# Performance work log

Measured on AMD Instinct MI355X. Metric: run time of the kernel, lower is better.

## Reference

```python
import jax, jax.numpy as jnp
import numpy as np

A = 4   # tree arity
D = 7   # tree depth; total nodes = (A**D - 1)//(A - 1) = 5461
B = 64  # batch size
E = 128 # embedding_dim
H = 128 # encode_dim
V = 50000
N_NODES = (A**D - 1) // (A - 1)


def setup_inputs() -> dict:
    key = jax.random.key(0)
    ks = jax.random.split(key, 9)
    tokens = jax.random.randint(ks[0], (N_NODES, B), 0, V, dtype=jnp.int64)
    emb = jax.random.normal(ks[1], (V, E), dtype=jnp.float32) * 0.05
    sent_w = jax.random.normal(ks[2], (H, H), dtype=jnp.float32) * 0.05
    sent_b = jax.random.normal(ks[3], (1, H), dtype=jnp.float32) * 0.05
    ctx_w = jax.random.normal(ks[4], (H, 1), dtype=jnp.float32) * 0.05
    w_ih = jax.random.normal(ks[5], (3 * H, E), dtype=jnp.float32) * 0.05
    w_hh = jax.random.normal(ks[6], (3 * H, H), dtype=jnp.float32) * 0.05
    b_ih = jax.random.normal(ks[7], (3 * H,), dtype=jnp.float32) * 0.05
    b_hh = jax.random.normal(ks[8], (3 * H,), dtype=jnp.float32) * 0.05
    return {"tokens": tokens, "emb": emb, "sent_w": sent_w, "sent_b": sent_b,
            "ctx_w": ctx_w, "w_ih": w_ih, "w_hh": w_hh, "b_ih": b_ih, "b_hh": b_hh}


def _gru_step(x, h, w_ih, w_hh, b_ih, b_hh):
    # x: [n, B, E], h: [n, B, H] -> new hidden [n, B, H]. PyTorch gate order r,z,n.
    gi = jnp.einsum('nbe,ge->nbg', x, w_ih) + b_ih   # [n, B, 3H]
    gh = jnp.einsum('nbh,gh->nbg', h, w_hh) + b_hh
    ir, iz, in_ = jnp.split(gi, 3, axis=-1)
    hr, hz, hn_ = jnp.split(gh, 3, axis=-1)
    r = jax.nn.sigmoid(ir + hr)
    z = jax.nn.sigmoid(iz + hz)
    n = jnp.tanh(in_ + r * hn_)
    return (1.0 - z) * n + z * h


def reference(tokens, emb, sent_w, sent_b, ctx_w, w_ih, w_hh, b_ih, b_hh):
    # Bottom-up over tree levels (level-order storage): level d occupies
    # tokens[(A**d-1)//(A-1) : ... + A**d]. Each node position covers the whole batch.
    hs = None       # hiddens of the level below: [A**(d+1), B, H]
    out_max = None  # running elementwise max over all node hiddens (node_list max)
    for d in range(D - 1, -1, -1):
        n = A ** d
        off = (A ** d - 1) // (A - 1)
        tok = tokens[off:off + n]          # [n, B]
        x = emb[tok]                       # [n, B, E]
        if hs is None:
            h0 = jnp.zeros((n, B, H), dtype=emb.dtype)  # leaves: no children
        else:
            ch = hs.reshape(n, A, B, H)    # children hiddens per parent
            # attention: tanh(ch @ W + b), tanh(. @ ctx), softmax over children
            u = jnp.tanh(jnp.einsum('nabh,hk->nabk', ch, sent_w) + sent_b)
            s = jnp.tanh(jnp.einsum('nabk,k->nab', u, ctx_w[:, 0]))  # [n, A, B]
            alpha = jax.nn.softmax(s, axis=1)                        # over A children
            h0 = jnp.einsum('nabh,nab->nbh', ch, alpha)              # weighted sum
        hn = _gru_step(x, h0, w_ih, w_hh, b_ih, b_hh)                # [n, B, H]
        lvl_max = hn.max(axis=0)                                     # [B, H]
        out_max = lvl_max if out_max is None else jnp.maximum(out_max, lvl_max)
        hs = hn
    return out_max  # [B, H]
```

## Files before the change

kernel.cpp:

```cpp
#include <hip/hip_runtime.h>
#include <cstdint>
#include <cstddef>


typedef short  bf16x8 __attribute__((ext_vector_type(8)));
typedef float  f32x4  __attribute__((ext_vector_type(4)));

#define WS_ACC    0u
#define WS_WIH    1048576u
#define WS_WHH    (WS_WIH + 98304u)
#define WS_SWT    (WS_WHH + 98304u)
#define WS_EMBB   (WS_SWT + 32768u)
#define WS_HLEAF  (WS_EMBB + 12800000u)
#define WS_HA     (WS_HLEAF + 12800000u)
#define WS_HB     (WS_HA + 4194304u)

__device__ __forceinline__ float sigm(float x)   { return 1.0f / (1.0f + __expf(-x)); }
__device__ __forceinline__ float tanhf_(float x) { return 1.0f - 2.0f / (1.0f + __expf(2.0f * x)); }

__device__ __forceinline__ unsigned short f2b(float f) {
  unsigned u = __float_as_uint(f);
  u += 0x7fffu + ((u >> 16) & 1u);
  return (unsigned short)(u >> 16);
}
__device__ __forceinline__ float b2f(unsigned short s) {
  return __uint_as_float(((unsigned)s) << 16);
}

__device__ __forceinline__ unsigned fenc(float f) {
  unsigned u = __float_as_uint(f);
  return (u & 0x80000000u) ? ~u : (u | 0x80000000u);
}
__device__ __forceinline__ float fdec(unsigned e) {
  unsigned u = (e & 0x80000000u) ? (e & 0x7fffffffu) : ~e;
  return __uint_as_float(u);
}

__device__ __forceinline__ f32x4 mfma16(bf16x8 a, bf16x8 b, f32x4 c) {
  return __builtin_amdgcn_mfma_f32_16x16x32_bf16(a, b, c, 0, 0, 0);
}

__global__ __launch_bounds__(256) void decode_out(const unsigned* __restrict__ acc,
                                                  float* __restrict__ out) {
  int i = blockIdx.x * 256 + threadIdx.x;
  unsigned m = 0u;
  for (int s = 0; s < 32; ++s) m = max(m, acc[s * 8192 + i]);
  out[i] = fdec(m);
}

__global__ __launch_bounds__(256) void prep_all(const float* __restrict__ emb,
                                                const float* __restrict__ wih,
                                                const float* __restrict__ whh,
                                                const float* __restrict__ sw,
                                                unsigned short* __restrict__ embb,
                                                unsigned short* __restrict__ wihb,
                                                unsigned short* __restrict__ whhb,
                                                unsigned short* __restrict__ swtb,
                                                unsigned* __restrict__ acc) {
  size_t idx = (size_t)blockIdx.x * 256 + threadIdx.x;
  if (idx < 1600000u) {
    float4 v = *(const float4*)(emb + idx * 4);
    ushort4 o; o.x = f2b(v.x); o.y = f2b(v.y); o.z = f2b(v.z); o.w = f2b(v.w);
    *(ushort4*)(embb + idx * 4) = o;
  } else if (idx < 1714688u) {
    int i = (int)(idx - 1600000u);
    if (i < 49152)       wihb[i] = f2b(wih[i]);
    else if (i < 98304)  whhb[i - 49152] = f2b(whh[i - 49152]);
    else { int j = i - 98304; int k = j >> 7, h = j & 127; swtb[j] = f2b(sw[h * 128 + k]); }
  } else {
    acc[idx - 1714688u] = 0u;
  }
}

__global__ __launch_bounds__(512, 2) void prep_hleaf(
    const unsigned short* __restrict__ embb,
    const unsigned short* __restrict__ wih,
    const float*          __restrict__ b_ih,
    const float*          __restrict__ b_hh,
    unsigned short*       __restrict__ H)
{
  __shared__ unsigned short lds[64 * 128];
  __shared__ unsigned short hvb[64 * 128];
  const int t = threadIdx.x;
  const int base = blockIdx.x * 64;

#pragma unroll
  for (int i = 0; i < 2; ++i) {
    int g = t + 512 * i;
    int m = g >> 4, c = g & 15;
    int v = base + m; if (v > 49999) v = 49999;
    uint4 vv = *(const uint4*)(embb + (size_t)v * 128 + c * 8);
    *(uint4*)(lds + m * 128 + ((c ^ (m & 15)) << 3)) = vv;
  }

  const int w = __builtin_amdgcn_readfirstlane(t >> 6);
  const int lane = t & 63, l = lane & 15, q = lane >> 4;
  const int j = w * 16 + l;

  bf16x8 Br[4], Bz[4], Bn[4];
#pragma unroll
  for (int ks = 0; ks < 4; ++ks) {
    const int ko = ks * 32 + q * 8;
    Br[ks] = *(const bf16x8*)(wih + (size_t)j * 128 + ko);
    Bz[ks] = *(const bf16x8*)(wih + (size_t)(128 + j) * 128 + ko);
    Bn[ks] = *(const bf16x8*)(wih + (size_t)(256 + j) * 128 + ko);
  }
  const float bR = b_ih[j] + b_hh[j];
  const float bZ = b_ih[128 + j] + b_hh[128 + j];
  const float bN = b_ih[256 + j];
  const float bH = b_hh[256 + j];

  f32x4 Cr[4] = {{0,0,0,0},{0,0,0,0},{0,0,0,0},{0,0,0,0}};
  f32x4 Cz[4] = {{0,0,0,0},{0,0,0,0},{0,0,0,0},{0,0,0,0}};
  f32x4 Cn[4] = {{0,0,0,0},{0,0,0,0},{0,0,0,0},{0,0,0,0}};
  __syncthreads();

#pragma unroll
  for (int ks = 0; ks < 4; ++ks) {
    bf16x8 A[4];
#pragma unroll
    for (int mt = 0; mt < 4; ++mt) {
      int m = mt * 16 + l, c = ks * 4 + q;
      A[mt] = *(const bf16x8*)(lds + m * 128 + (((c ^ l) & 15) << 3));
    }
#pragma unroll
    for (int mt = 0; mt < 4; ++mt) {
      Cr[mt] = mfma16(A[mt], Br[ks], Cr[mt]);
      Cz[mt] = mfma16(A[mt], Bz[ks], Cz[mt]);
      Cn[mt] = mfma16(A[mt], Bn[ks], Cn[mt]);
    }
  }

#pragma unroll
  for (int mt = 0; mt < 4; ++mt)
#pragma unroll
    for (int e = 0; e < 4; ++e) {
      int b = mt * 16 + q * 4 + e;
      float r  = sigm(Cr[mt][e] + bR);
      float z  = sigm(Cz[mt][e] + bZ);
      float nv = tanhf_(Cn[mt][e] + bN + r * bH);
      float hv = (1.0f - z) * nv;
      hvb[b * 128 + (j ^ (q << 4))] = f2b(hv);
    }
  __syncthreads();

#pragma unroll
  for (int i = 0; i < 2; ++i) {
    int g = t + 512 * i;
    int b = g >> 4, c8 = (g & 15) * 8;
    int qq = (b >> 2) & 3;
    if (base + b < 50000) {
      uint4 v = *(const uint4*)(hvb + b * 128 + (c8 ^ (qq << 4)));
      *(uint4*)(H + (size_t)(base + b) * 128 + c8) = v;
    }
  }
}

template <bool LEAF>
__global__ __launch_bounds__(512, 2) void attn_gru(
    const unsigned short* __restrict__ hch,
    const int*            __restrict__ tokc,
    const unsigned short* __restrict__ hleaf,
    const unsigned short* __restrict__ swt,
    const float*          __restrict__ sb,
    const float*          __restrict__ ctx,
    const int*            __restrict__ tok,
    const unsigned short* __restrict__ embb,
    const unsigned short* __restrict__ wih,
    const unsigned short* __restrict__ whh,
    const float*          __restrict__ b_ih,
    const float*          __restrict__ b_hh,
    unsigned short*       __restrict__ hout,
    unsigned*             __restrict__ acc)
{
  __shared__ unsigned short chs[256 * 128];
  __shared__ float spart[4][256];
  __shared__ float alf[256];
  unsigned short* const atile = chs;
  unsigned short* const hvb   = chs + 16384;

  const int p = blockIdx.x;
  const int t = threadIdx.x;

  const int sm0 = t >> 4,         sc0 = t & 15;
  const int sm1 = (t + 512) >> 4, sc1 = (t + 512) & 15;
  const int* tp = tok + p * 64;
  uint4 px0 = *(const uint4*)(embb + (size_t)tp[sm0] * 128 + sc0 * 8);
  uint4 px1 = *(const uint4*)(embb + (size_t)tp[sm1] * 128 + sc1 * 8);

  if constexpr (LEAF) {
    const int* tokp = tokc + p * 256;
#pragma unroll
    for (int i = 0; i < 8; ++i) {
      int g = t + 512 * i, m = g >> 4, c = g & 15;
      uint4 v = *(const uint4*)(hleaf + (size_t)tokp[m] * 128 + c * 8);
      *(uint4*)(chs + m * 128 + ((c ^ (m & 15)) << 3)) = v;
    }
  } else {
    const unsigned short* src = hch + (size_t)p * 256 * 128;
#pragma unroll
    for (int i = 0; i < 8; ++i) {
      int g = t + 512 * i, m = g >> 4, c = g & 15;
      uint4 v = *(const uint4*)(src + m * 128 + c * 8);
      *(uint4*)(chs + m * 128 + ((c ^ (m & 15)) << 3)) = v;
    }
  }

  const int w = __builtin_amdgcn_readfirstlane(t >> 6);
  const int wm = w >> 2, wn = w & 3;
  const int lane = t & 63, l = lane & 15, q = lane >> 4;
  const int j = w * 16 + l;

  bf16x8 Bs[2][4];
#pragma unroll
  for (int nt = 0; nt < 2; ++nt)
#pragma unroll
    for (int ks = 0; ks < 4; ++ks)
      Bs[nt][ks] = *(const bf16x8*)(swt + (size_t)(wn * 32 + nt * 16 + l) * 128 + ks * 32 + q * 8);

  f32x4 Cu[8][2] = {};
  __syncthreads();

#pragma unroll
  for (int ks = 0; ks < 4; ++ks) {
#pragma unroll
    for (int mt = 0; mt < 8; ++mt) {
      int m = wm * 128 + mt * 16 + l;
      int c = ks * 4 + q;
      bf16x8 A = *(const bf16x8*)(chs + m * 128 + (((c ^ (m & 15)) & 15) << 3));
      Cu[mt][0] = mfma16(A, Bs[0][ks], Cu[mt][0]);
      Cu[mt][1] = mfma16(A, Bs[1][ks], Cu[mt][1]);
    }
  }

  const float sb0 = sb[wn * 32 + l],  sb1 = sb[wn * 32 + 16 + l];
  const float cx0 = ctx[wn * 32 + l], cx1 = ctx[wn * 32 + 16 + l];
#pragma unroll
  for (int mt = 0; mt < 8; ++mt) {
    float pe[4];
#pragma unroll
    for (int e = 0; e < 4; ++e)
      pe[e] = tanhf_(Cu[mt][0][e] + sb0) * cx0 + tanhf_(Cu[mt][1][e] + sb1) * cx1;
#pragma unroll
    for (int mask = 1; mask < 16; mask <<= 1)
#pragma unroll
      for (int e = 0; e < 4; ++e)
        pe[e] += __shfl_xor(pe[e], mask, 16);
    if (l == 0) {
      int r = wm * 128 + mt * 16 + q * 4;
#pragma unroll
      for (int e = 0; e < 4; ++e) spart[wn][r + e] = pe[e];
    }
  }
  __syncthreads();

  if (t < 256) {
    float s = tanhf_(spart[0][t] + spart[1][t] + spart[2][t] + spart[3][t]);
    spart[0][t] = s;
  }
  __syncthreads();
  if (t < 64) {
    float s0 = spart[0][t], s1 = spart[0][64 + t], s2 = spart[0][128 + t], s3 = spart[0][192 + t];
    float m = fmaxf(fmaxf(s0, s1), fmaxf(s2, s3));
    float e0 = __expf(s0 - m), e1 = __expf(s1 - m), e2 = __expf(s2 - m), e3 = __expf(s3 - m);
    float inv = 1.0f / (e0 + e1 + e2 + e3);
    alf[t] = e0 * inv; alf[64 + t] = e1 * inv; alf[128 + t] = e2 * inv; alf[192 + t] = e3 * inv;
  }
  __syncthreads();

  float o[2][8];
#pragma unroll
  for (int i = 0; i < 2; ++i) {
    int id = t + 512 * i, b = id >> 4, c = id & 15;
#pragma unroll
    for (int k = 0; k < 8; ++k) o[i][k] = 0.0f;
#pragma unroll
    for (int a = 0; a < 4; ++a) {
      int m = a * 64 + b;
      const unsigned short* rp = chs + m * 128 + ((c ^ (m & 15)) << 3);
      float al = alf[m];
#pragma unroll
      for (int k = 0; k < 8; ++k) o[i][k] += al * b2f(rp[k]);
    }
  }

  float mxv[16];
  if constexpr (LEAF) {
    const int jj = t & 127, cc = jj >> 3;
#pragma unroll
    for (int e = 0; e < 16; ++e) mxv[e] = -1e30f;
#pragma unroll
    for (int a = 0; a < 4; ++a)
#pragma unroll
      for (int e = 0; e < 16; ++e) {
        int b = (t >> 7) + 4 * e, m = a * 64 + b;
        float v = b2f(chs[m * 128 + (((cc ^ (m & 15)) & 15) << 3) + (jj & 7)]);
        mxv[e] = fmaxf(mxv[e], v);
      }
  }
  __syncthreads();

  *(uint4*)(atile + sm0 * 256 + ((sc0 ^ (sm0 & 15)) << 3)) = px0;
  *(uint4*)(atile + sm1 * 256 + ((sc1 ^ (sm1 & 15)) << 3)) = px1;
#pragma unroll
  for (int i = 0; i < 2; ++i) {
    int id = t + 512 * i, b = id >> 4, c = id & 15;
    ushort4 h0a, h0b4;
    h0a.x = f2b(o[i][0]); h0a.y = f2b(o[i][1]); h0a.z = f2b(o[i][2]); h0a.w = f2b(o[i][3]);
    h0b4.x = f2b(o[i][4]); h0b4.y = f2b(o[i][5]); h0b4.z = f2b(o[i][6]); h0b4.w = f2b(o[i][7]);
    unsigned short* dst = atile + b * 256 + ((16 | ((c ^ (b & 15)) & 15)) << 3);
    *(ushort4*)dst = h0a;
    *(ushort4*)(dst + 4) = h0b4;
  }

  bf16x8 Br[8], Bz[8], Bn[4], Bh[4];
#pragma unroll
  for (int ks = 0; ks < 4; ++ks) {
    const int ko = ks * 32 + q * 8;
    Br[ks]     = *(const bf16x8*)(wih + (size_t)j * 128 + ko);
    Bz[ks]     = *(const bf16x8*)(wih + (size_t)(128 + j) * 128 + ko);
    Bn[ks]     = *(const bf16x8*)(wih + (size_t)(256 + j) * 128 + ko);
    Br[4 + ks] = *(const bf16x8*)(whh + (size_t)j * 128 + ko);
    Bz[4 + ks] = *(const bf16x8*)(whh + (size_t)(128 + j) * 128 + ko);
    Bh[ks]     = *(const bf16x8*)(whh + (size_t)(256 + j) * 128 + ko);
  }
  const float bR = b_ih[j] + b_hh[j];
  const float bZ = b_ih[128 + j] + b_hh[128 + j];
  const float bN = b_ih[256 + j];
  const float bH = b_hh[256 + j];
  __syncthreads();

  f32x4 Cr[4] = {{0,0,0,0},{0,0,0,0},{0,0,0,0},{0,0,0,0}};
  f32x4 Cz[4] = {{0,0,0,0},{0,0,0,0},{0,0,0,0},{0,0,0,0}};
  f32x4 Cn[4] = {{0,0,0,0},{0,0,0,0},{0,0,0,0},{0,0,0,0}};
  f32x4 Ch[4] = {{0,0,0,0},{0,0,0,0},{0,0,0,0},{0,0,0,0}};

#pragma unroll
  for (int ks = 0; ks < 8; ++ks) {
#pragma unroll
    for (int mt = 0; mt < 4; ++mt) {
      int m = mt * 16 + l;
      int c = ks * 4 + q;
      bf16x8 Amt = *(const bf16x8*)(atile + m * 256 + (((c & 16) | ((c ^ l) & 15)) << 3));
      Cr[mt] = mfma16(Amt, Br[ks], Cr[mt]);
      Cz[mt] = mfma16(Amt, Bz[ks], Cz[mt]);
      if (ks < 4) Cn[mt] = mfma16(Amt, Bn[ks], Cn[mt]);
      else        Ch[mt] = mfma16(Amt, Bh[ks - 4], Ch[mt]);
    }
  }

  float mx[4][4];
#pragma unroll
  for (int mt = 0; mt < 4; ++mt) {
#pragma unroll
    for (int e = 0; e < 4; ++e) {
      const int b = mt * 16 + q * 4 + e;
      float r  = sigm(Cr[mt][e] + bR);
      float z  = sigm(Cz[mt][e] + bZ);
      float nv = tanhf_(Cn[mt][e] + bN + r * (Ch[mt][e] + bH));
      int c16 = j >> 3;
      float hp = b2f(atile[b * 256 + ((16 | ((c16 ^ (b & 15)) & 15)) << 3) + (j & 7)]);
      float hv = (1.0f - z) * nv + z * hp;
      hvb[b * 128 + (j ^ (q << 4))] = f2b(hv);
      mx[mt][e] = hv;
    }
  }
  __syncthreads();

  unsigned short* ho = hout + (size_t)p * 8192;
  {
    int c80 = sc0 * 8, q0 = (sm0 >> 2) & 3;
    int c81 = sc1 * 8, q1 = (sm1 >> 2) & 3;
    uint4 v0 = *(const uint4*)(hvb + sm0 * 128 + (c80 ^ (q0 << 4)));
    uint4 v1 = *(const uint4*)(hvb + sm1 * 128 + (c81 ^ (q1 << 4)));
    *(uint4*)(ho + sm0 * 128 + c80) = v0;
    *(uint4*)(ho + sm1 * 128 + c81) = v1;
  }

  unsigned* accs = acc + (p & 31) * 8192;
#pragma unroll
  for (int mt = 0; mt < 4; ++mt)
#pragma unroll
    for (int e = 0; e < 4; ++e) {
      const int b = mt * 16 + q * 4 + e;
      atomicMax(accs + b * 128 + j, fenc(mx[mt][e]));
    }
  if constexpr (LEAF) {
#pragma unroll
    for (int e = 0; e < 16; ++e)
      atomicMax(accs + t + 512 * e, fenc(mxv[e]));
  }
}

extern "C" void kernel_launch(void* const* d_in, const int* in_sizes, int n_in,
                              void* d_out, int out_size, void* d_ws, size_t ws_size,
                              hipStream_t stream) {
  const int*   tokens = (const int*)d_in[0];
  const float* emb    = (const float*)d_in[1];
  const float* sent_w = (const float*)d_in[2];
  const float* sent_b = (const float*)d_in[3];
  const float* ctx_w  = (const float*)d_in[4];
  const float* w_ih   = (const float*)d_in[5];
  const float* w_hh   = (const float*)d_in[6];
  const float* b_ih   = (const float*)d_in[7];
  const float* b_hh   = (const float*)d_in[8];

  char* ws = (char*)d_ws;
  unsigned*       acc  = (unsigned*)(ws + WS_ACC);
  unsigned short* wihb = (unsigned short*)(ws + WS_WIH);
  unsigned short* whhb = (unsigned short*)(ws + WS_WHH);
  unsigned short* swtb = (unsigned short*)(ws + WS_SWT);
  unsigned short* embb = (unsigned short*)(ws + WS_EMBB);
  unsigned short* hlf  = (unsigned short*)(ws + WS_HLEAF);
  unsigned short* hA   = (unsigned short*)(ws + WS_HA);
  unsigned short* hB   = (unsigned short*)(ws + WS_HB);

  hipLaunchKernelGGL(prep_all, dim3(7722), dim3(256), 0, stream,
                     emb, w_ih, w_hh, sent_w, embb, wihb, whhb, swtb, acc);
  hipLaunchKernelGGL(prep_hleaf, dim3(782), dim3(512), 0, stream,
                     embb, wihb, b_ih, b_hh, hlf);

  static const int offs[7] = {0, 1, 5, 21, 85, 341, 1365};
  const int* tok6 = tokens + (size_t)1365 * 64;

  for (int d = 5; d >= 0; --d) {
    int n = 1 << (2 * d);
    unsigned short* hout  = (d & 1) ? hB : hA;
    unsigned short* child = (d & 1) ? hA : hB;
    if (d == 5) {
      hipLaunchKernelGGL((attn_gru<true>), dim3(n), dim3(512), 0, stream,
                         (const unsigned short*)nullptr, tok6, hlf,
                         swtb, sent_b, ctx_w,
                         tokens + (size_t)offs[5] * 64, embb, wihb, whhb,
                         b_ih, b_hh, hout, acc);
    } else {
      hipLaunchKernelGGL((attn_gru<false>), dim3(n), dim3(512), 0, stream,
                         child, (const int*)nullptr, (const unsigned short*)nullptr,
                         swtb, sent_b, ctx_w,
                         tokens + (size_t)offs[d] * 64, embb, wihb, whhb,
                         b_ih, b_hh, hout, acc);
    }
  }
  hipLaunchKernelGGL(decode_out, dim3(32), dim3(256), 0, stream, acc, (float*)d_out);
}
```

Baseline: 350.5 us.

## Split each tree node's batch across two blocks and raise occupancy

Each attn_gru block now handles half of the 64-wide batch for one parent node, which doubles the grid and halves the shared-memory tile (256x128 down to 128x128 bf16). Launch bounds go from 2 to 4 blocks per CU, and the GRU weight fragments are streamed with a one-step register prefetch instead of all being held in registers. The goal is more parallelism on the small upper tree levels and higher occupancy to hide memory latency. In exchange, the W_ih/W_hh and attention weights are reloaded by twice as many blocks, and register limits under the higher occupancy target could cause spills.

```diff
diff --git a/kernel.cpp b/kernel.cpp
--- a/kernel.cpp
+++ b/kernel.cpp
@@ -157,7 +157,7 @@
 }
 
 template <bool LEAF>
-__global__ __launch_bounds__(512, 2) void attn_gru(
+__global__ __launch_bounds__(512, 4) void attn_gru(
     const unsigned short* __restrict__ hch,
     const int*            __restrict__ tokc,
     const unsigned short* __restrict__ hleaf,
@@ -173,35 +173,35 @@
     unsigned short*       __restrict__ hout,
     unsigned*             __restrict__ acc)
 {
-  __shared__ unsigned short chs[256 * 128];
-  __shared__ float spart[4][256];
-  __shared__ float alf[256];
+  __shared__ unsigned short chs[128 * 128];
+  __shared__ float spart[4][128];
+  __shared__ float alf[128];
   unsigned short* const atile = chs;
-  unsigned short* const hvb   = chs + 16384;
-
-  const int p = blockIdx.x;
+  unsigned short* const hvb   = chs + 8192;
+
+  const int p2 = blockIdx.x;
+  const int p = p2 >> 1, half = p2 & 1;
   const int t = threadIdx.x;
 
-  const int sm0 = t >> 4,         sc0 = t & 15;
-  const int sm1 = (t + 512) >> 4, sc1 = (t + 512) & 15;
-  const int* tp = tok + p * 64;
-  uint4 px0 = *(const uint4*)(embb + (size_t)tp[sm0] * 128 + sc0 * 8);
-  uint4 px1 = *(const uint4*)(embb + (size_t)tp[sm1] * 128 + sc1 * 8);
+  const int sm = t >> 4, sc = t & 15;
+  const int* tp = tok + p * 64 + half * 32;
+  uint4 px = *(const uint4*)(embb + (size_t)tp[sm] * 128 + sc * 8);
 
   if constexpr (LEAF) {
     const int* tokp = tokc + p * 256;
 #pragma unroll
-    for (int i = 0; i < 8; ++i) {
+    for (int i = 0; i < 4; ++i) {
       int g = t + 512 * i, m = g >> 4, c = g & 15;
-      uint4 v = *(const uint4*)(hleaf + (size_t)tokp[m] * 128 + c * 8);
+      int bg = (m >> 5) * 64 + half * 32 + (m & 31);
+      uint4 v = *(const uint4*)(hleaf + (size_t)tokp[bg] * 128 + c * 8);
       *(uint4*)(chs + m * 128 + ((c ^ (m & 15)) << 3)) = v;
     }
   } else {
-    const unsigned short* src = hch + (size_t)p * 256 * 128;
-#pragma unroll
-    for (int i = 0; i < 8; ++i) {
+#pragma unroll
+    for (int i = 0; i < 4; ++i) {
       int g = t + 512 * i, m = g >> 4, c = g & 15;
-      uint4 v = *(const uint4*)(src + m * 128 + c * 8);
+      int bg = (m >> 5) * 64 + half * 32 + (m & 31);
+      uint4 v = *(const uint4*)(hch + ((size_t)p * 256 + bg) * 128 + c * 8);
       *(uint4*)(chs + m * 128 + ((c ^ (m & 15)) << 3)) = v;
     }
   }
@@ -218,14 +218,14 @@
     for (int ks = 0; ks < 4; ++ks)
       Bs[nt][ks] = *(const bf16x8*)(swt + (size_t)(wn * 32 + nt * 16 + l) * 128 + ks * 32 + q * 8);
 
-  f32x4 Cu[8][2] = {};
+  f32x4 Cu[4][2] = {};
   __syncthreads();
 
 #pragma unroll
   for (int ks = 0; ks < 4; ++ks) {
 #pragma unroll
-    for (int mt = 0; mt < 8; ++mt) {
-      int m = wm * 128 + mt * 16 + l;
+    for (int mt = 0; mt < 4; ++mt) {
+      int m = wm * 64 + mt * 16 + l;
       int c = ks * 4 + q;
       bf16x8 A = *(const bf16x8*)(chs + m * 128 + (((c ^ (m & 15)) & 15) << 3));
       Cu[mt][0] = mfma16(A, Bs[0][ks], Cu[mt][0]);
@@ -236,7 +236,7 @@
   const float sb0 = sb[wn * 32 + l],  sb1 = sb[wn * 32 + 16 + l];
   const float cx0 = ctx[wn * 32 + l], cx1 = ctx[wn * 32 + 16 + l];
 #pragma unroll
-  for (int mt = 0; mt < 8; ++mt) {
+  for (int mt = 0; mt < 4; ++mt) {
     float pe[4];
 #pragma unroll
     for (int e = 0; e < 4; ++e)
@@ -247,111 +247,110 @@
       for (int e = 0; e < 4; ++e)
         pe[e] += __shfl_xor(pe[e], mask, 16);
     if (l == 0) {
-      int r = wm * 128 + mt * 16 + q * 4;
+      int r = wm * 64 + mt * 16 + q * 4;
 #pragma unroll
       for (int e = 0; e < 4; ++e) spart[wn][r + e] = pe[e];
     }
   }
   __syncthreads();
 
-  if (t < 256) {
-    float s = tanhf_(spart[0][t] + spart[1][t] + spart[2][t] + spart[3][t]);
-    spart[0][t] = s;
-  }
-  __syncthreads();
-  if (t < 64) {
-    float s0 = spart[0][t], s1 = spart[0][64 + t], s2 = spart[0][128 + t], s3 = spart[0][192 + t];
-    float m = fmaxf(fmaxf(s0, s1), fmaxf(s2, s3));
-    float e0 = __expf(s0 - m), e1 = __expf(s1 - m), e2 = __expf(s2 - m), e3 = __expf(s3 - m);
+  if (t < 32) {
+    float sv[4];
+#pragma unroll
+    for (int a = 0; a < 4; ++a) {
+      int r = a * 32 + t;
+      sv[a] = tanhf_(spart[0][r] + spart[1][r] + spart[2][r] + spart[3][r]);
+    }
+    float m = fmaxf(fmaxf(sv[0], sv[1]), fmaxf(sv[2], sv[3]));
+    float e0 = __expf(sv[0] - m), e1 = __expf(sv[1] - m);
+    float e2 = __expf(sv[2] - m), e3 = __expf(sv[3] - m);
     float inv = 1.0f / (e0 + e1 + e2 + e3);
-    alf[t] = e0 * inv; alf[64 + t] = e1 * inv; alf[128 + t] = e2 * inv; alf[192 + t] = e3 * inv;
-  }
-  __syncthreads();
-
-  float o[2][8];
-#pragma unroll
-  for (int i = 0; i < 2; ++i) {
-    int id = t + 512 * i, b = id >> 4, c = id & 15;
-#pragma unroll
-    for (int k = 0; k < 8; ++k) o[i][k] = 0.0f;
+    alf[t] = e0 * inv; alf[32 + t] = e1 * inv; alf[64 + t] = e2 * inv; alf[96 + t] = e3 * inv;
+  }
+  __syncthreads();
+
+  float o[8] = {0, 0, 0, 0, 0, 0, 0, 0};
+  {
+    int rb = t >> 4, c = t & 15;
 #pragma unroll
     for (int a = 0; a < 4; ++a) {
-      int m = a * 64 + b;
+      int m = a * 32 + rb;
       const unsigned short* rp = chs + m * 128 + ((c ^ (m & 15)) << 3);
       float al = alf[m];
 #pragma unroll
-      for (int k = 0; k < 8; ++k) o[i][k] += al * b2f(rp[k]);
-    }
-  }
-
-  float mxv[16];
+      for (int k = 0; k < 8; ++k) o[k] += al * b2f(rp[k]);
+    }
+  }
+
+  float mxv[8];
   if constexpr (LEAF) {
     const int jj = t & 127, cc = jj >> 3;
 #pragma unroll
-    for (int e = 0; e < 16; ++e) mxv[e] = -1e30f;
+    for (int e = 0; e < 8; ++e) mxv[e] = -1e30f;
 #pragma unroll
     for (int a = 0; a < 4; ++a)
 #pragma unroll
-      for (int e = 0; e < 16; ++e) {
-        int b = (t >> 7) + 4 * e, m = a * 64 + b;
+      for (int e = 0; e < 8; ++e) {
+        int rb = (t >> 7) + 4 * e, m = a * 32 + rb;
         float v = b2f(chs[m * 128 + (((cc ^ (m & 15)) & 15) << 3) + (jj & 7)]);
         mxv[e] = fmaxf(mxv[e], v);
       }
   }
   __syncthreads();
 
-  *(uint4*)(atile + sm0 * 256 + ((sc0 ^ (sm0 & 15)) << 3)) = px0;
-  *(uint4*)(atile + sm1 * 256 + ((sc1 ^ (sm1 & 15)) << 3)) = px1;
-#pragma unroll
-  for (int i = 0; i < 2; ++i) {
-    int id = t + 512 * i, b = id >> 4, c = id & 15;
-    ushort4 h0a, h0b4;
-    h0a.x = f2b(o[i][0]); h0a.y = f2b(o[i][1]); h0a.z = f2b(o[i][2]); h0a.w = f2b(o[i][3]);
-    h0b4.x = f2b(o[i][4]); h0b4.y = f2b(o[i][5]); h0b4.z = f2b(o[i][6]); h0b4.w = f2b(o[i][7]);
-    unsigned short* dst = atile + b * 256 + ((16 | ((c ^ (b & 15)) & 15)) << 3);
-    *(ushort4*)dst = h0a;
-    *(ushort4*)(dst + 4) = h0b4;
-  }
-
-  bf16x8 Br[8], Bz[8], Bn[4], Bh[4];
-#pragma unroll
-  for (int ks = 0; ks < 4; ++ks) {
-    const int ko = ks * 32 + q * 8;
-    Br[ks]     = *(const bf16x8*)(wih + (size_t)j * 128 + ko);
-    Bz[ks]     = *(const bf16x8*)(wih + (size_t)(128 + j) * 128 + ko);
-    Bn[ks]     = *(const bf16x8*)(wih + (size_t)(256 + j) * 128 + ko);
-    Br[4 + ks] = *(const bf16x8*)(whh + (size_t)j * 128 + ko);
-    Bz[4 + ks] = *(const bf16x8*)(whh + (size_t)(128 + j) * 128 + ko);
-    Bh[ks]     = *(const bf16x8*)(whh + (size_t)(256 + j) * 128 + ko);
-  }
+  *(uint4*)(atile + sm * 256 + ((sc ^ (sm & 15)) << 3)) = px;
+  {
+    int rb = t >> 4, c = t & 15;
+    ushort4 ha, hb;
+    ha.x = f2b(o[0]); ha.y = f2b(o[1]); ha.z = f2b(o[2]); ha.w = f2b(o[3]);
+    hb.x = f2b(o[4]); hb.y = f2b(o[5]); hb.z = f2b(o[6]); hb.w = f2b(o[7]);
+    unsigned short* dst = atile + rb * 256 + ((16 | ((c ^ (rb & 15)) & 15)) << 3);
+    *(ushort4*)dst = ha;
+    *(ushort4*)(dst + 4) = hb;
+  }
+
+  const unsigned short* wI = wih + (size_t)j * 128 + q * 8;
+  const unsigned short* wH = whh + (size_t)j * 128 + q * 8;
   const float bR = b_ih[j] + b_hh[j];
   const float bZ = b_ih[128 + j] + b_hh[128 + j];
   const float bN = b_ih[256 + j];
   const float bH = b_hh[256 + j];
   __syncthreads();
 
-  f32x4 Cr[4] = {{0,0,0,0},{0,0,0,0},{0,0,0,0},{0,0,0,0}};
-  f32x4 Cz[4] = {{0,0,0,0},{0,0,0,0},{0,0,0,0},{0,0,0,0}};
-  f32x4 Cn[4] = {{0,0,0,0},{0,0,0,0},{0,0,0,0},{0,0,0,0}};
-  f32x4 Ch[4] = {{0,0,0,0},{0,0,0,0},{0,0,0,0},{0,0,0,0}};
+  f32x4 Cr[2] = {{0,0,0,0},{0,0,0,0}};
+  f32x4 Cz[2] = {{0,0,0,0},{0,0,0,0}};
+  f32x4 Cn[2] = {{0,0,0,0},{0,0,0,0}};
+  f32x4 Ch[2] = {{0,0,0,0},{0,0,0,0}};
+
+  bf16x8 b0 = *(const bf16x8*)(wI);
+  bf16x8 b1 = *(const bf16x8*)(wI + 128 * 128);
+  bf16x8 b2 = *(const bf16x8*)(wI + 256 * 128);
 
 #pragma unroll
   for (int ks = 0; ks < 8; ++ks) {
-#pragma unroll
-    for (int mt = 0; mt < 4; ++mt) {
+    bf16x8 c0 = b0, c1 = b1, c2 = b2;
+    if (ks + 1 < 8) {
+      const unsigned short* base = (ks + 1 >= 4) ? wH : wI;
+      const int ko = ((ks + 1) & 3) * 32;
+      b0 = *(const bf16x8*)(base + ko);
+      b1 = *(const bf16x8*)(base + 128 * 128 + ko);
+      b2 = *(const bf16x8*)(base + 256 * 128 + ko);
+    }
+#pragma unroll
+    for (int mt = 0; mt < 2; ++mt) {
       int m = mt * 16 + l;
       int c = ks * 4 + q;
       bf16x8 Amt = *(const bf16x8*)(atile + m * 256 + (((c & 16) | ((c ^ l) & 15)) << 3));
-      Cr[mt] = mfma16(Amt, Br[ks], Cr[mt]);
-      Cz[mt] = mfma16(Amt, Bz[ks], Cz[mt]);
-      if (ks < 4) Cn[mt] = mfma16(Amt, Bn[ks], Cn[mt]);
-      else        Ch[mt] = mfma16(Amt, Bh[ks - 4], Ch[mt]);
-    }
-  }
-
-  float mx[4][4];
-#pragma unroll
-  for (int mt = 0; mt < 4; ++mt) {
+      Cr[mt] = mfma16(Amt, c0, Cr[mt]);
+      Cz[mt] = mfma16(Amt, c1, Cz[mt]);
+      if (ks < 4) Cn[mt] = mfma16(Amt, c2, Cn[mt]);
+      else        Ch[mt] = mfma16(Amt, c2, Ch[mt]);
+    }
+  }
+
+  float mx[2][4];
+#pragma unroll
+  for (int mt = 0; mt < 2; ++mt) {
 #pragma unroll
     for (int e = 0; e < 4; ++e) {
       const int b = mt * 16 + q * 4 + e;
@@ -367,28 +366,24 @@
   }
   __syncthreads();
 
-  unsigned short* ho = hout + (size_t)p * 8192;
   {
-    int c80 = sc0 * 8, q0 = (sm0 >> 2) & 3;
-    int c81 = sc1 * 8, q1 = (sm1 >> 2) & 3;
-    uint4 v0 = *(const uint4*)(hvb + sm0 * 128 + (c80 ^ (q0 << 4)));
-    uint4 v1 = *(const uint4*)(hvb + sm1 * 128 + (c81 ^ (q1 << 4)));
-    *(uint4*)(ho + sm0 * 128 + c80) = v0;
-    *(uint4*)(ho + sm1 * 128 + c81) = v1;
-  }
-
-  unsigned* accs = acc + (p & 31) * 8192;
-#pragma unroll
-  for (int mt = 0; mt < 4; ++mt)
+    int qq = (sm >> 2) & 3;
+    uint4 v = *(const uint4*)(hvb + sm * 128 + ((sc * 8) ^ (qq << 4)));
+    *(uint4*)(hout + ((size_t)p * 64 + half * 32 + sm) * 128 + sc * 8) = v;
+  }
+
+  unsigned* accs = acc + (p2 & 31) * 8192;
+#pragma unroll
+  for (int mt = 0; mt < 2; ++mt)
 #pragma unroll
     for (int e = 0; e < 4; ++e) {
-      const int b = mt * 16 + q * 4 + e;
-      atomicMax(accs + b * 128 + j, fenc(mx[mt][e]));
+      const int bg = half * 32 + mt * 16 + q * 4 + e;
+      atomicMax(accs + bg * 128 + j, fenc(mx[mt][e]));
     }
   if constexpr (LEAF) {
 #pragma unroll
-    for (int e = 0; e < 16; ++e)
-      atomicMax(accs + t + 512 * e, fenc(mxv[e]));
+    for (int e = 0; e < 8; ++e)
+      atomicMax(accs + half * 4096 + t + 512 * e, fenc(mxv[e]));
   }
 }
 
@@ -428,13 +423,13 @@
     unsigned short* hout  = (d & 1) ? hB : hA;
     unsigned short* child = (d & 1) ? hA : hB;
     if (d == 5) {
-      hipLaunchKernelGGL((attn_gru<true>), dim3(n), dim3(512), 0, stream,
+      hipLaunchKernelGGL((attn_gru<true>), dim3(2 * n), dim3(512), 0, stream,
                          (const unsigned short*)nullptr, tok6, hlf,
                          swtb, sent_b, ctx_w,
                          tokens + (size_t)offs[5] * 64, embb, wihb, whhb,
                          b_ih, b_hh, hout, acc);
     } else {
-      hipLaunchKernelGGL((attn_gru<false>), dim3(n), dim3(512), 0, stream,
+      hipLaunchKernelGGL((attn_gru<false>), dim3(2 * n), dim3(512), 0, stream,
                          child, (const int*)nullptr, (const unsigned short*)nullptr,
                          swtb, sent_b, ctx_w,
                          tokens + (size_t)offs[d] * 64, embb, wihb, whhb,
```

Result: faster. 309.4 us (-11.7%).
